# Kernel tuning notes

Hardware: AMD Instinct MI355X
Metric: run time of the kernel (lower is better)

The kernel has to match this reference:

```python
import jax, jax.numpy as jnp
import numpy as np

R = 32           # voxel resolution
NEG_SLOPE = 0.1  # LeakyReLU slope in PVCNN voxel layers
BN_EPS = 1e-4    # BatchNorm3d eps used by PVCNN


def _voxelize(features, coords):
    # features [B,C,N], coords [B,3,N]; normalize=True, eps=0
    B, C, N = features.shape
    norm = coords - coords.mean(axis=2, keepdims=True)
    scale = jnp.linalg.norm(norm, axis=1).max(axis=1)        # [B] max point radius
    norm = norm / (scale[:, None, None] * 2.0) + 0.5         # -> roughly [0,1]
    norm = jnp.clip(norm * R, 0.0, R - 1)                    # float coords in [0,R-1]
    v = jnp.round(norm).astype(jnp.int32)                    # [B,3,N]
    idx = (v[:, 0] * R + v[:, 1]) * R + v[:, 2]              # [B,N] flat voxel index

    def scatter_avg(f, i):  # f [C,N], i [N]
        cnt = jnp.zeros((R ** 3,), f.dtype).at[i].add(1.0)
        s = jnp.zeros((f.shape[0], R ** 3), f.dtype).at[:, i].add(f)
        return s / jnp.maximum(cnt, 1.0)

    grid = jax.vmap(scatter_avg)(features, idx).reshape(B, C, R, R, R)
    return grid, norm


def _devoxelize(grid, coords):
    # grid [B,C,R,R,R], coords float [B,3,N] in [0, R-1]
    B, C = grid.shape[:2]
    flat = grid.reshape(B, C, R ** 3)
    lo = jnp.floor(coords).astype(jnp.int32)
    f = coords - lo
    hi = jnp.minimum(lo + 1, R - 1)
    x0, y0, z0 = lo[:, 0], lo[:, 1], lo[:, 2]
    x1, y1, z1 = hi[:, 0], hi[:, 1], hi[:, 2]
    fx, fy, fz = f[:, 0], f[:, 1], f[:, 2]

    def corner(ix, iy, iz, w):
        idx = (ix * R + iy) * R + iz                          # [B,N]
        g = jax.vmap(lambda gf, ii: gf[:, ii])(flat, idx)     # [B,C,N]
        return g * w[:, None, :]

    return (corner(x0, y0, z0, (1 - fx) * (1 - fy) * (1 - fz))
            + corner(x0, y0, z1, (1 - fx) * (1 - fy) * fz)
            + corner(x0, y1, z0, (1 - fx) * fy * (1 - fz))
            + corner(x0, y1, z1, (1 - fx) * fy * fz)
            + corner(x1, y0, z0, fx * (1 - fy) * (1 - fz))
            + corner(x1, y0, z1, fx * (1 - fy) * fz)
            + corner(x1, y1, z0, fx * fy * (1 - fz))
            + corner(x1, y1, z1, fx * fy * fz))


def _conv_bn_lrelu(x, w, b, gamma, beta, mean, var):
    y = jax.lax.conv_general_dilated(
        x, w, window_strides=(1, 1, 1), padding='SAME',
        dimension_numbers=('NCDHW', 'OIDHW', 'NCDHW'))
    y = y + b[None, :, None, None, None]
    scale = gamma / jnp.sqrt(var + BN_EPS)
    y = (y - mean[None, :, None, None, None]) * scale[None, :, None, None, None] \
        + beta[None, :, None, None, None]
    return jnp.where(y >= 0, y, NEG_SLOPE * y)


def setup_inputs() -> dict:
    key = jax.random.key(0)
    ks = jax.random.split(key, 16)
    B, C, N = 8, 64, 65536
    inp = {
        'features': jax.random.normal(ks[0], (B, C, N), jnp.float32),
        'coords': jax.random.normal(ks[1], (B, 3, N), jnp.float32),
        'w1': jax.random.normal(ks[2], (64, 64, 3, 3, 3), jnp.float32) * 0.05,
        'b1': jax.random.normal(ks[3], (64,), jnp.float32) * 0.05,
        'g1': jax.random.uniform(ks[4], (64,), jnp.float32) + 0.5,
        'be1': jax.random.normal(ks[5], (64,), jnp.float32) * 0.1,
        'm1': jax.random.normal(ks[6], (64,), jnp.float32) * 0.1,
        'v1': jax.random.uniform(ks[7], (64,), jnp.float32) + 0.5,
        'w2': jax.random.normal(ks[8], (64, 64, 3, 3, 3), jnp.float32) * 0.05,
        'b2': jax.random.normal(ks[9], (64,), jnp.float32) * 0.05,
        'g2': jax.random.uniform(ks[10], (64,), jnp.float32) + 0.5,
        'be2': jax.random.normal(ks[11], (64,), jnp.float32) * 0.1,
        'm2': jax.random.normal(ks[12], (64,), jnp.float32) * 0.1,
        'v2': jax.random.uniform(ks[13], (64,), jnp.float32) + 0.5,
    }
    return inp


def reference(features, coords, w1, b1, g1, be1, m1, v1,
              w2, b2, g2, be2, m2, v2):
    grid, vox_coords = _voxelize(features, coords)           # [B,C,R,R,R], [B,3,N]
    grid = _conv_bn_lrelu(grid, w1, b1, g1, be1, m1, v1)
    grid = _conv_bn_lrelu(grid, w2, b2, g2, be2, m2, v2)
    point_feats = _devoxelize(grid, vox_coords)              # [B,Cout,N]
    return (point_feats, coords)
```

## Files before the change

### kernel.cpp

```cpp
#include <hip/hip_runtime.h>
#include <hip/hip_bf16.h>
#include <hip/hip_fp16.h>

#define NPTS   65536
#define BATCH  8
#define CH     64
#define RES    32
#define RCELLS 32768
#define NEG_SLOPE 0.1f
#define BN_EPS 1e-4f
#define GSPLIT 4

typedef float    f32x4 __attribute__((ext_vector_type(4)));
typedef _Float16 f16x8 __attribute__((ext_vector_type(8)));
typedef _Float16 f16x4 __attribute__((ext_vector_type(4)));

#define OFF_SUMS   0
#define OFF_SCALE  24
#define OFF_CNT    32
#define OFF_IDX    (OFF_CNT + BATCH*RCELLS)
#define OFF_CSTART (OFF_IDX + BATCH*NPTS)
#define OFF_ORDER  (OFF_CSTART + BATCH*RCELLS)
#define OFF_BN     (OFF_ORDER + BATCH*NPTS)
#define OFF_WP1    (OFF_BN + 256)
#define OFF_WP2    (OFF_WP1 + 55296)
#define OFF_FT     (OFF_WP2 + 55296)
#define OFF_GA     (OFF_FT + 16777216)
#define OFF_GB     (OFF_GA + 8388608)
#define OFF_META   OFF_FT

__device__ inline float waveReduceSum(float v) {
#pragma unroll
    for (int off = 32; off > 0; off >>= 1) v += __shfl_down(v, off, 64);
    return v;
}
__device__ inline float waveReduceMax(float v) {
#pragma unroll
    for (int off = 32; off > 0; off >>= 1) v = fmaxf(v, __shfl_down(v, off, 64));
    return v;
}

__global__ __launch_bounds__(256) void k_stats_sum(const float* __restrict__ coords,
                                                   float* __restrict__ sums) {
    __shared__ float sm[3][4];
    int b = blockIdx.x >> 3, chunk = blockIdx.x & 7;
    const float* cb = coords + (size_t)b * 3 * NPTS;
    float s0 = 0.f, s1 = 0.f, s2 = 0.f;
    for (int i = threadIdx.x; i < 8192; i += 256) {
        int n = chunk * 8192 + i;
        s0 += cb[n];
        s1 += cb[n + NPTS];
        s2 += cb[n + 2 * NPTS];
    }
    s0 = waveReduceSum(s0); s1 = waveReduceSum(s1); s2 = waveReduceSum(s2);
    int lane = threadIdx.x & 63, wid = threadIdx.x >> 6;
    if (lane == 0) { sm[0][wid] = s0; sm[1][wid] = s1; sm[2][wid] = s2; }
    __syncthreads();
    if (threadIdx.x == 0) {
        atomicAdd(&sums[b * 3 + 0], sm[0][0] + sm[0][1] + sm[0][2] + sm[0][3]);
        atomicAdd(&sums[b * 3 + 1], sm[1][0] + sm[1][1] + sm[1][2] + sm[1][3]);
        atomicAdd(&sums[b * 3 + 2], sm[2][0] + sm[2][1] + sm[2][2] + sm[2][3]);
    }
}

__global__ __launch_bounds__(256) void k_stats_max(const float* __restrict__ coords,
                                                   const float* __restrict__ sums,
                                                   unsigned int* __restrict__ scaleBits) {
    __shared__ float sm[4];
    int b = blockIdx.x >> 3, chunk = blockIdx.x & 7;
    const float* cb = coords + (size_t)b * 3 * NPTS;
    float mx = sums[b * 3 + 0] * (1.f / NPTS);
    float my = sums[b * 3 + 1] * (1.f / NPTS);
    float mz = sums[b * 3 + 2] * (1.f / NPTS);
    float m = 0.f;
    for (int i = threadIdx.x; i < 8192; i += 256) {
        int n = chunk * 8192 + i;
        float dx = cb[n] - mx, dy = cb[n + NPTS] - my, dz = cb[n + 2 * NPTS] - mz;
        m = fmaxf(m, sqrtf(dx * dx + dy * dy + dz * dz));
    }
    m = waveReduceMax(m);
    int lane = threadIdx.x & 63, wid = threadIdx.x >> 6;
    if (lane == 0) sm[wid] = m;
    __syncthreads();
    if (threadIdx.x == 0) {
        float r = fmaxf(fmaxf(sm[0], sm[1]), fmaxf(sm[2], sm[3]));
        atomicMax(&scaleBits[b], __float_as_uint(r));
    }
}

__global__ __launch_bounds__(256) void k_vox_assign(const float* __restrict__ coords,
                                                    const float* __restrict__ sums,
                                                    const unsigned int* __restrict__ scaleBits,
                                                    int* __restrict__ idxb,
                                                    int* __restrict__ cnt) {
    int g = blockIdx.x * 256 + threadIdx.x;
    int b = g >> 16, n = g & (NPTS - 1);
    const float* cb = coords + (size_t)b * 3 * NPTS;
    float scale2 = __uint_as_float(scaleBits[b]) * 2.f;
    int v[3];
#pragma unroll
    for (int d = 0; d < 3; ++d) {
        float mean = sums[b * 3 + d] * (1.f / NPTS);
        float x = (cb[d * NPTS + n] - mean) / scale2 + 0.5f;
        x *= (float)RES;
        x = fminf(fmaxf(x, 0.f), (float)(RES - 1));
        v[d] = (int)rintf(x);
    }
    int id = (v[0] * RES + v[1]) * RES + v[2];
    idxb[b * NPTS + n] = id;
    atomicAdd(&cnt[b * RCELLS + id], 1);
}

__global__ __launch_bounds__(256) void k_scan(const int* __restrict__ cnt,
                                              int* __restrict__ cellStart) {
    __shared__ int bufA[256], bufB[256];
    int b = blockIdx.x, tid = threadIdx.x;
    const int* cb = cnt + b * RCELLS;
    int sum = 0;
    for (int i = 0; i < 128; ++i) sum += cb[tid * 128 + i];
    bufA[tid] = sum;
    __syncthreads();
    int* src = bufA; int* dst = bufB;
    for (int off = 1; off < 256; off <<= 1) {
        int v = src[tid];
        if (tid >= off) v += src[tid - off];
        dst[tid] = v;
        __syncthreads();
        int* t = src; src = dst; dst = t;
    }
    int run = (tid > 0) ? src[tid - 1] : 0;
    int* cs = cellStart + b * RCELLS;
    for (int i = 0; i < 128; ++i) {
        int c = cb[tid * 128 + i];
        cs[tid * 128 + i] = run;
        run += c;
    }
}

__global__ __launch_bounds__(256) void k_rank(const int* __restrict__ idxb,
                                              int* __restrict__ cellStart,
                                              int* __restrict__ order) {
    int g = blockIdx.x * 256 + threadIdx.x;
    int b = g >> 16, n = g & (NPTS - 1);
    int cell = idxb[b * NPTS + n];
    int pos = atomicAdd(&cellStart[b * RCELLS + cell], 1);
    order[b * NPTS + pos] = n;
}

__global__ __launch_bounds__(256) void k_transpose(const float* __restrict__ f,
                                                   _Float16* __restrict__ featT) {
    int g = blockIdx.x * 256 + threadIdx.x;
    int b = g >> 16, n = g & (NPTS - 1);
    const float* fb = f + (size_t)b * CH * NPTS + n;
    _Float16* dst = featT + (size_t)g * 64;
#pragma unroll
    for (int k = 0; k < 8; ++k) {
        f16x8 hv;
#pragma unroll
        for (int j = 0; j < 8; ++j)
            hv[j] = (_Float16)fb[(size_t)(k * 8 + j) * NPTS];
        *(f16x8*)(dst + k * 8) = hv;
    }
}

__global__ __launch_bounds__(256) void k_gather(const _Float16* __restrict__ featT,
                                                const int* __restrict__ order,
                                                const int* __restrict__ cellStart,
                                                const int* __restrict__ cnt,
                                                _Float16* __restrict__ gA) {
    int bi = blockIdx.x;
    int b  = bi & 7;
    int chunk = bi >> 3;
    int r  = chunk * 256 + threadIdx.x;
    int sub  = r & (GSPLIT - 1);
    int ct   = (r >> 2) & 1;
    int cell = r >> 3;

    int e0 = cellStart[b * RCELLS + cell];
    int c  = cnt[b * RCELLS + cell];
    int s0 = e0 - c;
    int len = (c + GSPLIT - 1) >> 2;
    int s = s0 + sub * len;
    int e = min(s + len, e0);

    float acc[32];
#pragma unroll
    for (int j = 0; j < 32; ++j) acc[j] = 0.f;
    const int* ob = order + b * NPTS;
    const _Float16* fb = featT + (((size_t)b << 16)) * 64 + ct * 32;

    int p = s;
    for (; p + 8 <= e; p += 8) {
        int n[8];
#pragma unroll
        for (int u = 0; u < 8; ++u) n[u] = ob[p + u];
        f16x8 v[8][4];
#pragma unroll
        for (int u = 0; u < 8; ++u) {
            const _Float16* q = fb + (size_t)n[u] * 64;
#pragma unroll
            for (int k = 0; k < 4; ++k)
                v[u][k] = *(const f16x8*)(q + k * 8);
        }
#pragma unroll
        for (int u = 0; u < 8; ++u)
#pragma unroll
            for (int k = 0; k < 4; ++k)
#pragma unroll
                for (int j = 0; j < 8; ++j)
                    acc[k * 8 + j] += (float)v[u][k][j];
    }
    for (; p < e; ++p) {
        int n = ob[p];
        const _Float16* q = fb + (size_t)n * 64;
#pragma unroll
        for (int k = 0; k < 4; ++k) {
            f16x8 vv = *(const f16x8*)(q + k * 8);
#pragma unroll
            for (int j = 0; j < 8; ++j)
                acc[k * 8 + j] += (float)vv[j];
        }
    }

#pragma unroll
    for (int j = 0; j < 32; ++j) {
        acc[j] += __shfl_xor(acc[j], 1, 64);
        acc[j] += __shfl_xor(acc[j], 2, 64);
    }

    if (sub == 0) {
        float inv = 1.f / (float)max(c, 1);
        _Float16* dst = gA + ((size_t)(b * 2 + ct) * RCELLS + cell) * 32;
#pragma unroll
        for (int k = 0; k < 4; ++k) {
            f16x8 hv;
#pragma unroll
            for (int j = 0; j < 8; ++j)
                hv[j] = (_Float16)(acc[k * 8 + j] * inv);
            *(f16x8*)(dst + k * 8) = hv;
        }
    }
}

__global__ __launch_bounds__(256) void k_prep(const float* __restrict__ w,
                                              const float* __restrict__ bias,
                                              const float* __restrict__ g,
                                              const float* __restrict__ be,
                                              const float* __restrict__ m,
                                              const float* __restrict__ v,
                                              _Float16* __restrict__ wP,
                                              float* __restrict__ bnA,
                                              float* __restrict__ bnB) {
    int s = blockIdx.x * 256 + threadIdx.x;
    int ci_in = s & 31;
    int t  = s >> 5;
    int co = t & 63;
    int tc = t >> 6;
    int ct = tc & 1;
    int tap = tc >> 1;
    int ci = ct * 32 + ci_in;
    wP[s] = (_Float16)w[co * 1728 + ci * 27 + tap];
    if (s < 64) {
        float A = g[s] / sqrtf(v[s] + BN_EPS);
        bnA[s] = A;
        bnB[s] = (bias[s] - m[s]) * A + be[s];
    }
}

__global__ __launch_bounds__(256, 2) void k_conv(const _Float16* __restrict__ gIn,
                                                 _Float16* __restrict__ gOut,
                                                 const _Float16* __restrict__ wP,
                                                 const float* __restrict__ bnA,
                                                 const float* __restrict__ bnB) {
    __shared__ _Float16 sIn[3 * 10 * 34 * 32];
    int bi = blockIdx.x;
    int b  = bi >> 7;
    int rem = bi & 127;
    int z  = rem >> 2;
    int yg = rem & 3;
    int tid = threadIdx.x;
    int wid = tid >> 6;
    int lane = tid & 63;
    int l15 = lane & 15, quad = lane >> 4;

    f32x4 acc[4][4];
#pragma unroll
    for (int mt = 0; mt < 4; ++mt)
#pragma unroll
        for (int nt = 0; nt < 4; ++nt) acc[mt][nt] = (f32x4){0.f, 0.f, 0.f, 0.f};

    const f16x8* wp8 = (const f16x8*)wP;

    int bbase[4];
#pragma unroll
    for (int nt = 0; nt < 4; ++nt) {
        int yl = 2 * wid + (nt >> 1);
        int x  = ((nt & 1) << 4) + l15;
        bbase[nt] = ((10 + (yl + 1)) * 34 + (x + 1)) * 32 + quad * 8;
    }

    for (int ct = 0; ct < 2; ++ct) {
        const _Float16* gin = gIn + (size_t)(b * 2 + ct) * (RCELLS * 32);
#pragma unroll
        for (int it = 0; it < 16; ++it) {
            int s = tid + it * 256;
            if (s < 4080) {
                int cc  = s & 3;
                int pos = s >> 2;
                int xx  = pos % 34;
                int t2  = pos / 34;
                int yy  = t2 % 10;
                int zz  = t2 / 10;
                int x = xx - 1, y = yg * 8 + yy - 1, z0 = z + zz - 1;
                f32x4 val = {0.f, 0.f, 0.f, 0.f};
                if ((unsigned)x < 32u && (unsigned)y < 32u && (unsigned)z0 < 32u)
                    val = *(const f32x4*)(gin + ((size_t)((z0 * 32 + y) * 32 + x)) * 32 + cc * 8);
                *(f32x4*)(sIn + (size_t)s * 8) = val;
            }
        }
        __syncthreads();

#pragma unroll
        for (int dz = -1; dz <= 1; ++dz)
#pragma unroll
        for (int dy = -1; dy <= 1; ++dy)
#pragma unroll
        for (int dx = -1; dx <= 1; ++dx) {
            int tap = (dz + 1) * 9 + (dy + 1) * 3 + (dx + 1);
            f16x8 aF[4];
#pragma unroll
            for (int mt = 0; mt < 4; ++mt)
                aF[mt] = wp8[tap * 512 + ct * 256 + mt * 64 + l15 * 4 + quad];
            f16x8 bF[4];
            int off = ((dz + 1) * 340 + dy * 34 + dx) * 32 - 340 * 32;
#pragma unroll
            for (int nt = 0; nt < 4; ++nt)
                bF[nt] = *(const f16x8*)(sIn + bbase[nt] + off);
#pragma unroll
            for (int mt = 0; mt < 4; ++mt)
#pragma unroll
                for (int nt = 0; nt < 4; ++nt)
                    acc[mt][nt] = __builtin_amdgcn_mfma_f32_16x16x32_f16(
                        aF[mt], bF[nt], acc[mt][nt], 0, 0, 0);
        }
        __syncthreads();
    }

#pragma unroll
    for (int nt = 0; nt < 4; ++nt) {
        int y = yg * 8 + 2 * wid + (nt >> 1);
        int x = ((nt & 1) << 4) + l15;
        int cell = z * 1024 + y * 32 + x;
#pragma unroll
        for (int mt = 0; mt < 4; ++mt) {
            int cob = mt * 16 + quad * 4;
            f32x4 An = *(const f32x4*)(bnA + cob);
            f32x4 Bn = *(const f32x4*)(bnB + cob);
            f16x4 hv;
#pragma unroll
            for (int r = 0; r < 4; ++r) {
                float t = acc[mt][nt][r] * An[r] + Bn[r];
                t = (t >= 0.f) ? t : NEG_SLOPE * t;
                hv[r] = (_Float16)t;
            }
            _Float16* op = gOut + ((size_t)(b * 2 + (cob >> 5)) * RCELLS + cell) * 32 + (cob & 31);
            *(f16x4*)op = hv;
        }
    }
}

__global__ __launch_bounds__(256) void k_dprep(const float* __restrict__ coords,
                                               const float* __restrict__ sums,
                                               const unsigned int* __restrict__ scaleBits,
                                               f32x4* __restrict__ meta) {
    int g = blockIdx.x * 256 + threadIdx.x;
    int b = g >> 16, n = g & (NPTS - 1);
    const float* cb = coords + (size_t)b * 3 * NPTS;
    float scale2 = __uint_as_float(scaleBits[b]) * 2.f;
    float nc[3];
#pragma unroll
    for (int d = 0; d < 3; ++d) {
        float mean = sums[b * 3 + d] * (1.f / NPTS);
        float x = (cb[d * NPTS + n] - mean) / scale2 + 0.5f;
        x *= (float)RES;
        nc[d] = fminf(fmaxf(x, 0.f), (float)(RES - 1));
    }
    float lx = floorf(nc[0]), ly = floorf(nc[1]), lz = floorf(nc[2]);
    int x0 = (int)lx, y0 = (int)ly, z0 = (int)lz;
    int dx = (x0 + 1 <= RES - 1) ? 1 : 0;
    int dy = (y0 + 1 <= RES - 1) ? 1 : 0;
    int dz = (z0 + 1 <= RES - 1) ? 1 : 0;
    int id0 = (x0 * RES + y0) * RES + z0;
    int pk = id0 | (dx << 15) | (dy << 16) | (dz << 17);
    f32x4 m;
    m[0] = nc[0] - lx; m[1] = nc[1] - ly; m[2] = nc[2] - lz;
    m[3] = __int_as_float(pk);
    meta[(size_t)b * NPTS + n] = m;
}

__global__ __launch_bounds__(256) void k_devox(const _Float16* __restrict__ gA,
                                               const f32x4* __restrict__ meta,
                                               float* __restrict__ out) {
    int w = blockIdx.x * 4 + (threadIdx.x >> 6);
    int lane = threadIdx.x & 63;
    int psub = lane & 15;
    int chunk = lane >> 4;
    int ct = w & 1;
    int group = w >> 1;
    int b = group >> 12;
    int n0 = (group & 4095) << 4;
    int n = n0 + psub;

    f32x4 m = meta[(size_t)b * NPTS + n];
    float fx = m[0], fy = m[1], fz = m[2];
    int pk = __float_as_int(m[3]);
    int id0 = pk & 32767;
    int xo = ((pk >> 15) & 1) << 10;
    int yo = ((pk >> 16) & 1) << 5;
    int zo = (pk >> 17) & 1;
    float gx = 1.f - fx, gy = 1.f - fy, gz = 1.f - fz;

    const _Float16* gb = gA + (size_t)(b * 2 + ct) * (RCELLS * 32) + chunk * 8;

    float acc[8];
#pragma unroll
    for (int j = 0; j < 8; ++j) acc[j] = 0.f;

#pragma unroll
    for (int c = 0; c < 8; ++c) {
        int id = id0 + ((c & 4) ? xo : 0) + ((c & 2) ? yo : 0) + ((c & 1) ? zo : 0);
        float wgt = ((c & 4) ? fx : gx) * ((c & 2) ? fy : gy) * ((c & 1) ? fz : gz);
        f16x8 v = *(const f16x8*)(gb + (size_t)id * 32);
#pragma unroll
        for (int j = 0; j < 8; ++j)
            acc[j] += wgt * (float)v[j];
    }

    float* ob = out + (size_t)b * CH * NPTS + (size_t)(ct * 32 + chunk * 8) * NPTS + n;
#pragma unroll
    for (int j = 0; j < 8; ++j)
        __builtin_nontemporal_store(acc[j], ob + (size_t)j * NPTS);
}

extern "C" void kernel_launch(void* const* d_in, const int* in_sizes, int n_in,
                              void* d_out, int out_size, void* d_ws, size_t ws_size,
                              hipStream_t stream) {
    const float* features = (const float*)d_in[0];
    const float* coords   = (const float*)d_in[1];
    const float* w1  = (const float*)d_in[2];
    const float* b1  = (const float*)d_in[3];
    const float* g1  = (const float*)d_in[4];
    const float* be1 = (const float*)d_in[5];
    const float* m1  = (const float*)d_in[6];
    const float* v1  = (const float*)d_in[7];
    const float* w2  = (const float*)d_in[8];
    const float* b2  = (const float*)d_in[9];
    const float* g2  = (const float*)d_in[10];
    const float* be2 = (const float*)d_in[11];
    const float* m2  = (const float*)d_in[12];
    const float* v2  = (const float*)d_in[13];

    float* ws = (float*)d_ws;
    float*        sums      = ws + OFF_SUMS;
    unsigned int* scaleBits = (unsigned int*)(ws + OFF_SCALE);
    int*          cnt       = (int*)(ws + OFF_CNT);
    int*          idxb      = (int*)(ws + OFF_IDX);
    int*          cellStart = (int*)(ws + OFF_CSTART);
    int*          order     = (int*)(ws + OFF_ORDER);
    float*        bnA1      = ws + OFF_BN;
    float*        bnB1      = ws + OFF_BN + 64;
    float*        bnA2      = ws + OFF_BN + 128;
    float*        bnB2      = ws + OFF_BN + 192;
    _Float16*     wP1       = (_Float16*)(ws + OFF_WP1);
    _Float16*     wP2       = (_Float16*)(ws + OFF_WP2);
    _Float16*     featT     = (_Float16*)(ws + OFF_FT);
    f32x4*        meta      = (f32x4*)(ws + OFF_META);
    _Float16*     gA        = (_Float16*)(ws + OFF_GA);
    _Float16*     gB        = (_Float16*)(ws + OFF_GB);

    (void)hipMemsetAsync(ws, 0, (size_t)(OFF_IDX) * sizeof(float), stream);

    k_stats_sum<<<64, 256, 0, stream>>>(coords, sums);
    k_stats_max<<<64, 256, 0, stream>>>(coords, sums, scaleBits);
    k_vox_assign<<<(BATCH * NPTS) / 256, 256, 0, stream>>>(coords, sums, scaleBits,
                                                           idxb, cnt);
    k_scan<<<BATCH, 256, 0, stream>>>(cnt, cellStart);
    k_rank<<<(BATCH * NPTS) / 256, 256, 0, stream>>>(idxb, cellStart, order);
    k_transpose<<<(BATCH * NPTS) / 256, 256, 0, stream>>>(features, featT);
    k_gather<<<(BATCH * RCELLS * 2 * GSPLIT) / 256, 256, 0, stream>>>(
        featT, order, cellStart, cnt, gA);
    k_prep<<<432, 256, 0, stream>>>(w1, b1, g1, be1, m1, v1, wP1, bnA1, bnB1);
    k_prep<<<432, 256, 0, stream>>>(w2, b2, g2, be2, m2, v2, wP2, bnA2, bnB2);
    k_conv<<<BATCH * RES * 4, 256, 0, stream>>>(gA, gB, wP1, bnA1, bnB1);
    k_dprep<<<(BATCH * NPTS) / 256, 256, 0, stream>>>(coords, sums, scaleBits, meta);
    k_conv<<<BATCH * RES * 4, 256, 0, stream>>>(gB, gA, wP2, bnA2, bnB2);
    k_devox<<<(2 * BATCH * NPTS / 16) / 4, 256, 0, stream>>>(gA, meta, (float*)d_out);

    (void)hipMemcpyAsync((float*)d_out + (size_t)BATCH * CH * NPTS, coords,
                         (size_t)BATCH * 3 * NPTS * sizeof(float),
                         hipMemcpyDeviceToDevice, stream);
}
```

Measured before the change: 692.7 us.

## Prefetch second channel-tile halo into registers during first tile's MFMA compute

Halo-tile offsets for the shared-memory load are now computed once into per-thread arrays, instead of being recomputed with div/mod on every channel-tile iteration. The global loads for the second channel group are issued into 16 registers right after the first tile is staged, so their latency overlaps with the first group's MFMA work, and they are then written to LDS. This adds about 64 extra VGPRs for the prefetch buffer plus 32 offset registers. Under launch_bounds(256,2) that could cause spills or lower occupancy.

Result: faster. 672.9 us (-2.9%).

```diff
diff --git a/kernel.cpp b/kernel.cpp
--- a/kernel.cpp
+++ b/kernel.cpp
@@ -283,13 +283,42 @@
     int lane = tid & 63;
     int l15 = lane & 15, quad = lane >> 4;
 
+    int soff[16], goff[16];
+#pragma unroll
+    for (int it = 0; it < 16; ++it) {
+        int s = tid + it * 256;
+        soff[it] = -1; goff[it] = -1;
+        if (s < 4080) {
+            int cc  = s & 3;
+            int pos = s >> 2;
+            int xx  = pos % 34;
+            int t2  = pos / 34;
+            int yy  = t2 % 10;
+            int zz  = t2 / 10;
+            int x = xx - 1, y = yg * 8 + yy - 1, z0 = z + zz - 1;
+            soff[it] = s * 8;
+            if ((unsigned)x < 32u && (unsigned)y < 32u && (unsigned)z0 < 32u)
+                goff[it] = ((z0 * 32 + y) * 32 + x) * 32 + cc * 8;
+        }
+    }
+
+    const _Float16* gin0 = gIn + (size_t)(b * 2) * (RCELLS * 32);
+    const _Float16* gin1 = gin0 + (size_t)RCELLS * 32;
+
+#pragma unroll
+    for (int it = 0; it < 16; ++it) {
+        if (soff[it] >= 0) {
+            f32x4 val = {0.f, 0.f, 0.f, 0.f};
+            if (goff[it] >= 0) val = *(const f32x4*)(gin0 + goff[it]);
+            *(f32x4*)(sIn + soff[it]) = val;
+        }
+    }
+
     f32x4 acc[4][4];
 #pragma unroll
     for (int mt = 0; mt < 4; ++mt)
 #pragma unroll
         for (int nt = 0; nt < 4; ++nt) acc[mt][nt] = (f32x4){0.f, 0.f, 0.f, 0.f};
-
-    const f16x8* wp8 = (const f16x8*)wP;
 
     int bbase[4];
 #pragma unroll
@@ -299,26 +328,27 @@
         bbase[nt] = ((10 + (yl + 1)) * 34 + (x + 1)) * 32 + quad * 8;
     }
 
+    __syncthreads();
+
+    f32x4 pre[16];
+#pragma unroll
+    for (int it = 0; it < 16; ++it) {
+        f32x4 val = {0.f, 0.f, 0.f, 0.f};
+        if (goff[it] >= 0) val = *(const f32x4*)(gin1 + goff[it]);
+        pre[it] = val;
+    }
+
+    const f16x8* wp8 = (const f16x8*)wP;
+
+#pragma unroll
     for (int ct = 0; ct < 2; ++ct) {
-        const _Float16* gin = gIn + (size_t)(b * 2 + ct) * (RCELLS * 32);
-#pragma unroll
-        for (int it = 0; it < 16; ++it) {
-            int s = tid + it * 256;
-            if (s < 4080) {
-                int cc  = s & 3;
-                int pos = s >> 2;
-                int xx  = pos % 34;
-                int t2  = pos / 34;
-                int yy  = t2 % 10;
-                int zz  = t2 / 10;
-                int x = xx - 1, y = yg * 8 + yy - 1, z0 = z + zz - 1;
-                f32x4 val = {0.f, 0.f, 0.f, 0.f};
-                if ((unsigned)x < 32u && (unsigned)y < 32u && (unsigned)z0 < 32u)
-                    val = *(const f32x4*)(gin + ((size_t)((z0 * 32 + y) * 32 + x)) * 32 + cc * 8);
-                *(f32x4*)(sIn + (size_t)s * 8) = val;
-            }
-        }
-        __syncthreads();
+        if (ct == 1) {
+            __syncthreads();
+#pragma unroll
+            for (int it = 0; it < 16; ++it)
+                if (soff[it] >= 0) *(f32x4*)(sIn + soff[it]) = pre[it];
+            __syncthreads();
+        }
 
 #pragma unroll
         for (int dz = -1; dz <= 1; ++dz)
@@ -343,7 +373,6 @@
                     acc[mt][nt] = __builtin_amdgcn_mfma_f32_16x16x32_f16(
                         aF[mt], bF[nt], acc[mt][nt], 0, 0, 0);
         }
-        __syncthreads();
     }
 
 #pragma unroll
```
